# Optimization experiments

Hardware: AMD Instinct MI355X
Metric: run time of the kernel (lower is better)

The kernel has to match this reference:

```python
import jax, jax.numpy as jnp
import numpy as np

NUM_CLASSES = 10
GAMMA = 1.0
EPS = 1e-12


def setup_inputs() -> dict:
    key = jax.random.key(0)
    k1, k2, k3, k4 = jax.random.split(key, 4)
    x = jax.random.normal(k1, (1024, 64), dtype=jnp.float32)
    exemplars = jax.random.normal(k2, (50000, 64), dtype=jnp.float32)
    exemplar_labels = jax.random.randint(k3, (50000,), 0, NUM_CLASSES)
    # beta_raw initialized as softplus^{-1}(init_beta) with init_beta=1.0
    init_beta = 1.0
    beta_raw = jnp.array([np.log(np.exp(init_beta) - 1.0)], dtype=jnp.float32)
    return {"x": x, "exemplars": exemplars, "exemplar_labels": exemplar_labels,
            "beta_raw": beta_raw}


def reference(x, exemplars, exemplar_labels, beta_raw):
    # Squared Euclidean distances (weight_diag == ones) via GEMM expansion:
    # d2[b, e] = ||x_b||^2 + ||e_e||^2 - 2 <x_b, e_e>
    x2 = jnp.sum(x * x, axis=-1, keepdims=True)            # (B, 1)
    e2 = jnp.sum(exemplars * exemplars, axis=-1)           # (Ne,)
    d2 = x2 + e2[None, :] - 2.0 * (x @ exemplars.T)        # (B, Ne)
    d2 = jnp.maximum(d2, 0.0)  # true sq-dist is nonneg; guards GEMM round-off
    beta = jax.nn.softplus(beta_raw[0])
    sims = jnp.exp(-beta * d2)                              # (B, Ne)
    # scatter-add similarities into per-class bins: (C, B) -> (B, C)
    class_sims = jax.ops.segment_sum(sims.T, exemplar_labels,
                                     num_segments=NUM_CLASSES).T
    logits = GAMMA * jnp.log(class_sims + EPS)
    return logits
```

## Files before the change

### kernel.cpp

```cpp
#include <hip/hip_runtime.h>


#define NB      1024
#define NE      50000
#define NE_PAD  50176
#define NCHUNK  196
#define CROWS   256
#define KD      64
#define NC      10
#define SROWS   64
#define NSTAGE  4

using half8   = __attribute__((ext_vector_type(8))) _Float16;
using half4v  = __attribute__((ext_vector_type(4))) _Float16;
using floatx4 = __attribute__((ext_vector_type(4))) float;

__device__ __forceinline__ float softplus_f(float x) {
  return (x > 20.f) ? x : log1pf(__expf(x));
}

__global__ __launch_bounds__(256) void prep_kernel(
    const float* __restrict__ x, const float* __restrict__ ex,
    const int* __restrict__ labels, const float* __restrict__ beta_raw,
    _Float16* __restrict__ ex_h, float* __restrict__ ce,
    _Float16* __restrict__ x_h, float* __restrict__ cb,
    _Float16* __restrict__ oh_pre)
{
  const int tid = threadIdx.x;
  const float beta = softplus_f(beta_raw[0]);

  const int row = blockIdx.x * 16 + (tid >> 4);
  const int l16 = tid & 15;

  if (row < NE_PAD) {
    float4 v = make_float4(0.f, 0.f, 0.f, 0.f);
    if (row < NE) v = ((const float4*)ex)[row * 16 + l16];
    half4v hv = { (_Float16)v.x, (_Float16)v.y, (_Float16)v.z, (_Float16)v.w };
    *(half4v*)(ex_h + (size_t)row * KD + l16 * 4) = hv;
    float s = v.x*v.x + v.y*v.y + v.z*v.z + v.w*v.w;
    #pragma unroll
    for (int m = 1; m < 16; m <<= 1) s += __shfl_xor(s, m, 64);
    if (l16 == 0) ce[row] = (row < NE) ? (-beta * s) : -1e30f;
  } else {
    const int rx = row - NE_PAD;
    float4 v = ((const float4*)x)[rx * 16 + l16];
    half4v hv = { (_Float16)v.x, (_Float16)v.y, (_Float16)v.z, (_Float16)v.w };
    *(half4v*)(x_h + (size_t)rx * KD + l16 * 4) = hv;
    float s = v.x*v.x + v.y*v.y + v.z*v.z + v.w*v.w;
    #pragma unroll
    for (int m = 1; m < 16; m <<= 1) s += __shfl_xor(s, m, 64);
    if (l16 == 0) cb[rx] = -beta * s;
  }

  if (blockIdx.x < (NE_PAD / 16) && tid < 64) {
    const int l15  = tid & 15;
    const int quad = tid >> 4;
    const int base = min(blockIdx.x * 16 + quad * 4, NE - 4);
    const int4 lb = *(const int4*)(labels + base);
    half4v oh;
    oh[0] = (lb.x == l15) ? (_Float16)1.f : (_Float16)0.f;
    oh[1] = (lb.y == l15) ? (_Float16)1.f : (_Float16)0.f;
    oh[2] = (lb.z == l15) ? (_Float16)1.f : (_Float16)0.f;
    oh[3] = (lb.w == l15) ? (_Float16)1.f : (_Float16)0.f;
    ((half4v*)oh_pre)[blockIdx.x * 64 + tid] = oh;
  }
}

__global__ __launch_bounds__(256) void main_kernel(
    const _Float16* __restrict__ ex_h, const float* __restrict__ ce,
    const _Float16* __restrict__ x_h, const float* __restrict__ cb,
    const _Float16* __restrict__ oh_pre, const float* __restrict__ beta_raw,
    float* __restrict__ part)
{
  __shared__ _Float16 Ah[2][SROWS * KD];

  const int tid  = threadIdx.x;
  const int wave = tid >> 6;
  const int lane = tid & 63;
  const int l15  = lane & 15;
  const int quad = lane >> 4;

  const int btile = blockIdx.x;
  const int chunk = blockIdx.y;
  const int e0    = chunk * CROWS;
  const int bm    = btile * 128 + wave * 32;

  const float beta = softplus_f(beta_raw[0]);
  const float s2 = 2.f * beta;

  const half8* xr0 = (const half8*)(x_h + (size_t)(bm + l15) * KD);
  const half8* xr1 = (const half8*)(x_h + (size_t)(bm + 16 + l15) * KD);
  const half8 bx00 = xr0[quad];
  const half8 bx01 = xr0[quad + 4];
  const half8 bx10 = xr1[quad];
  const half8 bx11 = xr1[quad + 4];
  const float cbl0 = cb[bm + l15];
  const float cbl1 = cb[bm + 16 + l15];

  const int srow = tid >> 2;
  const int scol = tid & 3;
  const int ssw  = srow & 7;
  const _Float16* gsrc = ex_h + (size_t)(e0 + srow) * KD + scol * 16;
  const int lofs0 = srow * KD + (((2 * scol)     ^ ssw) * 8);
  const int lofs1 = srow * KD + (((2 * scol + 1) ^ ssw) * 8);

  half8 pr0 = *(const half8*)(gsrc);
  half8 pr1 = *(const half8*)(gsrc + 8);
  *(half8*)(&Ah[0][lofs0]) = pr0;
  *(half8*)(&Ah[0][lofs1]) = pr1;
  __syncthreads();

  floatx4 acc0 = {0.f, 0.f, 0.f, 0.f};
  floatx4 acc1 = {0.f, 0.f, 0.f, 0.f};

  const int rsw = l15 & 7;

  #pragma unroll
  for (int st = 0; st < NSTAGE; ++st) {
    const int b = st & 1;

    if (st + 1 < NSTAGE) {
      const _Float16* g = gsrc + (size_t)(st + 1) * SROWS * KD;
      pr0 = *(const half8*)(g);
      pr1 = *(const half8*)(g + 8);
    }

    float4 ce4s[4]; half4v ohs[4];
    #pragma unroll
    for (int sub = 0; sub < 4; ++sub) {
      ce4s[sub] = *(const float4*)(ce + e0 + st * SROWS + sub * 16 + quad * 4);
      ohs[sub]  = ((const half4v*)oh_pre)[(size_t)(chunk * 16 + st * 4 + sub) * 64 + lane];
    }

    #pragma unroll
    for (int sub = 0; sub < 4; ++sub) {
      const int rs = sub * 16 + l15;
      const half8 ae0 = *(const half8*)(&Ah[b][rs * KD + ((quad ^ rsw) * 8)]);
      const half8 ae1 = *(const half8*)(&Ah[b][rs * KD + (((quad + 4) ^ rsw) * 8)]);

      floatx4 d0 = {0.f, 0.f, 0.f, 0.f};
      d0 = __builtin_amdgcn_mfma_f32_16x16x32_f16(ae0, bx00, d0, 0, 0, 0);
      d0 = __builtin_amdgcn_mfma_f32_16x16x32_f16(ae1, bx01, d0, 0, 0, 0);
      floatx4 d1 = {0.f, 0.f, 0.f, 0.f};
      d1 = __builtin_amdgcn_mfma_f32_16x16x32_f16(ae0, bx10, d1, 0, 0, 0);
      d1 = __builtin_amdgcn_mfma_f32_16x16x32_f16(ae1, bx11, d1, 0, 0, 0);

      const float4 ce4 = ce4s[sub];
      const float cef[4] = { ce4.x, ce4.y, ce4.z, ce4.w };
      half4v p0, p1;
      #pragma unroll
      for (int r = 0; r < 4; ++r) {
        const float t0 = fminf(fmaf(s2, d0[r], cbl0 + cef[r]), 0.f);
        const float t1 = fminf(fmaf(s2, d1[r], cbl1 + cef[r]), 0.f);
        p0[r] = (_Float16)__expf(t0);
        p1[r] = (_Float16)__expf(t1);
      }

      acc0 = __builtin_amdgcn_mfma_f32_16x16x16f16(ohs[sub], p0, acc0, 0, 0, 0);
      acc1 = __builtin_amdgcn_mfma_f32_16x16x16f16(ohs[sub], p1, acc1, 0, 0, 0);
    }

    if (st + 1 < NSTAGE) {
      __syncthreads();
      const int nb = (st + 1) & 1;
      *(half8*)(&Ah[nb][lofs0]) = pr0;
      *(half8*)(&Ah[nb][lofs1]) = pr1;
      __syncthreads();
    }
  }

  float* dst = part + (size_t)chunk * (NB * NC);
  #pragma unroll
  for (int r = 0; r < 4; ++r) {
    const int c = quad * 4 + r;
    if (c < NC) {
      dst[(bm + l15) * NC + c]      = acc0[r];
      dst[(bm + 16 + l15) * NC + c] = acc1[r];
    }
  }
}

__global__ __launch_bounds__(256) void reduce_kernel(
    const float* __restrict__ part, float* __restrict__ out)
{
  const int bc = blockIdx.x * 256 + threadIdx.x;
  if (bc < NB * NC) {
    float s = 0.f;
    #pragma unroll 7
    for (int k = 0; k < NCHUNK; ++k) s += part[(size_t)k * (NB * NC) + bc];
    out[bc] = __logf(s + 1e-12f);
  }
}

extern "C" void kernel_launch(void* const* d_in, const int* in_sizes, int n_in,
                              void* d_out, int out_size, void* d_ws, size_t ws_size,
                              hipStream_t stream)
{
  const float* x        = (const float*)d_in[0];
  const float* ex       = (const float*)d_in[1];
  const int*   labels   = (const int*)d_in[2];
  const float* beta_raw = (const float*)d_in[3];
  float* out = (float*)d_out;

  char* ws = (char*)d_ws;
  _Float16* ex_h   = (_Float16*)ws;
  float*    ce     = (float*)(ws + 6422528);
  _Float16* x_h    = (_Float16*)(ws + 6623232);
  float*    cb     = (float*)(ws + 6754304);
  _Float16* oh_pre = (_Float16*)(ws + 6758400);
  float*    part   = (float*)(ws + 8364032);

  prep_kernel<<<3200, 256, 0, stream>>>(x, ex, labels, beta_raw,
                                        ex_h, ce, x_h, cb, oh_pre);
  dim3 g(8, 196);
  main_kernel<<<g, 256, 0, stream>>>(ex_h, ce, x_h, cb, oh_pre, beta_raw, part);
  reduce_kernel<<<40, 256, 0, stream>>>(part, out);
}
```

Before: 108.1 us.

## Load whole exemplar chunk to LDS once and widen per-wave batch tile

The main kernel now loads the full 256-row exemplar chunk, its norms and its one-hot labels into shared memory in a single pass with one barrier. The staged double-buffer loop and its per-stage barriers are gone. Each wave now covers 64 batch rows instead of 32, and the grid shrinks from 1568 to 784 blocks. This halves redundant exemplar reloads across batch tiles and removes synchronisation, at the cost of more registers, more LDS per block, fewer blocks and no load/compute overlap.

New measurement: 107.3 us. No clear change (-0.7%).

```diff
diff --git a/kernel.cpp b/kernel.cpp
--- a/kernel.cpp
+++ b/kernel.cpp
@@ -8,8 +8,6 @@
 #define CROWS   256
 #define KD      64
 #define NC      10
-#define SROWS   64
-#define NSTAGE  4
 
 using half8   = __attribute__((ext_vector_type(8))) _Float16;
 using half4v  = __attribute__((ext_vector_type(4))) _Float16;
@@ -72,7 +70,9 @@
     const _Float16* __restrict__ oh_pre, const float* __restrict__ beta_raw,
     float* __restrict__ part)
 {
-  __shared__ _Float16 Ah[2][SROWS * KD];
+  __shared__ _Float16 Ah[CROWS * KD];
+  __shared__ float    CeS[CROWS];
+  __shared__ _Float16 OhS[16 * 64 * 4];
 
   const int tid  = threadIdx.x;
   const int wave = tid >> 6;
@@ -80,102 +80,87 @@
   const int l15  = lane & 15;
   const int quad = lane >> 4;
 
-  const int btile = blockIdx.x;
-  const int chunk = blockIdx.y;
+  const int chunk = blockIdx.x >> 2;
+  const int grp   = blockIdx.x & 3;
   const int e0    = chunk * CROWS;
-  const int bm    = btile * 128 + wave * 32;
+  const int bmw   = grp * 256 + wave * 64;
 
   const float beta = softplus_f(beta_raw[0]);
   const float s2 = 2.f * beta;
 
-  const half8* xr0 = (const half8*)(x_h + (size_t)(bm + l15) * KD);
-  const half8* xr1 = (const half8*)(x_h + (size_t)(bm + 16 + l15) * KD);
-  const half8 bx00 = xr0[quad];
-  const half8 bx01 = xr0[quad + 4];
-  const half8 bx10 = xr1[quad];
-  const half8 bx11 = xr1[quad + 4];
-  const float cbl0 = cb[bm + l15];
-  const float cbl1 = cb[bm + 16 + l15];
-
   const int srow = tid >> 2;
   const int scol = tid & 3;
-  const int ssw  = srow & 7;
   const _Float16* gsrc = ex_h + (size_t)(e0 + srow) * KD + scol * 16;
-  const int lofs0 = srow * KD + (((2 * scol)     ^ ssw) * 8);
-  const int lofs1 = srow * KD + (((2 * scol + 1) ^ ssw) * 8);
-
-  half8 pr0 = *(const half8*)(gsrc);
-  half8 pr1 = *(const half8*)(gsrc + 8);
-  *(half8*)(&Ah[0][lofs0]) = pr0;
-  *(half8*)(&Ah[0][lofs1]) = pr1;
+  half8 r0[4], r1[4];
+  #pragma unroll
+  for (int p = 0; p < 4; ++p) {
+    r0[p] = *(const half8*)(gsrc + (size_t)p * 64 * KD);
+    r1[p] = *(const half8*)(gsrc + (size_t)p * 64 * KD + 8);
+  }
+  const float cev = ce[e0 + tid];
+  const int4* ohg = (const int4*)((const char*)oh_pre + (size_t)chunk * 8192 + tid * 32);
+  const int4 oha = ohg[0];
+  const int4 ohb = ohg[1];
+
+  half8 bx0[4], bx1[4];
+  float cbl[4];
+  #pragma unroll
+  for (int g2 = 0; g2 < 4; ++g2) {
+    const half8* xr = (const half8*)(x_h + (size_t)(bmw + g2 * 16 + l15) * KD);
+    bx0[g2] = xr[quad];
+    bx1[g2] = xr[quad + 4];
+    cbl[g2] = cb[bmw + g2 * 16 + l15];
+  }
+
+  const int ssw = srow & 7;
+  #pragma unroll
+  for (int p = 0; p < 4; ++p) {
+    const int rr = p * 64 + srow;
+    *(half8*)(&Ah[rr * KD + (((2 * scol)     ^ ssw) * 8)]) = r0[p];
+    *(half8*)(&Ah[rr * KD + (((2 * scol + 1) ^ ssw) * 8)]) = r1[p];
+  }
+  CeS[tid] = cev;
+  ((int4*)OhS)[tid * 2]     = oha;
+  ((int4*)OhS)[tid * 2 + 1] = ohb;
   __syncthreads();
 
-  floatx4 acc0 = {0.f, 0.f, 0.f, 0.f};
-  floatx4 acc1 = {0.f, 0.f, 0.f, 0.f};
-
+  floatx4 acc[4] = { {0,0,0,0}, {0,0,0,0}, {0,0,0,0}, {0,0,0,0} };
   const int rsw = l15 & 7;
 
-  #pragma unroll
-  for (int st = 0; st < NSTAGE; ++st) {
-    const int b = st & 1;
-
-    if (st + 1 < NSTAGE) {
-      const _Float16* g = gsrc + (size_t)(st + 1) * SROWS * KD;
-      pr0 = *(const half8*)(g);
-      pr1 = *(const half8*)(g + 8);
-    }
-
-    float4 ce4s[4]; half4v ohs[4];
-    #pragma unroll
-    for (int sub = 0; sub < 4; ++sub) {
-      ce4s[sub] = *(const float4*)(ce + e0 + st * SROWS + sub * 16 + quad * 4);
-      ohs[sub]  = ((const half4v*)oh_pre)[(size_t)(chunk * 16 + st * 4 + sub) * 64 + lane];
-    }
-
-    #pragma unroll
-    for (int sub = 0; sub < 4; ++sub) {
-      const int rs = sub * 16 + l15;
-      const half8 ae0 = *(const half8*)(&Ah[b][rs * KD + ((quad ^ rsw) * 8)]);
-      const half8 ae1 = *(const half8*)(&Ah[b][rs * KD + (((quad + 4) ^ rsw) * 8)]);
-
-      floatx4 d0 = {0.f, 0.f, 0.f, 0.f};
-      d0 = __builtin_amdgcn_mfma_f32_16x16x32_f16(ae0, bx00, d0, 0, 0, 0);
-      d0 = __builtin_amdgcn_mfma_f32_16x16x32_f16(ae1, bx01, d0, 0, 0, 0);
-      floatx4 d1 = {0.f, 0.f, 0.f, 0.f};
-      d1 = __builtin_amdgcn_mfma_f32_16x16x32_f16(ae0, bx10, d1, 0, 0, 0);
-      d1 = __builtin_amdgcn_mfma_f32_16x16x32_f16(ae1, bx11, d1, 0, 0, 0);
-
-      const float4 ce4 = ce4s[sub];
-      const float cef[4] = { ce4.x, ce4.y, ce4.z, ce4.w };
-      half4v p0, p1;
+  #pragma unroll 4
+  for (int rsub = 0; rsub < 16; ++rsub) {
+    const int rs = rsub * 16 + l15;
+    const half8 ae0 = *(const half8*)(&Ah[rs * KD + ((quad ^ rsw) * 8)]);
+    const half8 ae1 = *(const half8*)(&Ah[rs * KD + (((quad + 4) ^ rsw) * 8)]);
+    const float4 ce4 = *(const float4*)(&CeS[rsub * 16 + quad * 4]);
+    const half4v oh  = ((const half4v*)OhS)[rsub * 64 + lane];
+    const float cef[4] = { ce4.x, ce4.y, ce4.z, ce4.w };
+
+    #pragma unroll
+    for (int g2 = 0; g2 < 4; ++g2) {
+      floatx4 d = {0.f, 0.f, 0.f, 0.f};
+      d = __builtin_amdgcn_mfma_f32_16x16x32_f16(ae0, bx0[g2], d, 0, 0, 0);
+      d = __builtin_amdgcn_mfma_f32_16x16x32_f16(ae1, bx1[g2], d, 0, 0, 0);
+
+      half4v p;
       #pragma unroll
       for (int r = 0; r < 4; ++r) {
-        const float t0 = fminf(fmaf(s2, d0[r], cbl0 + cef[r]), 0.f);
-        const float t1 = fminf(fmaf(s2, d1[r], cbl1 + cef[r]), 0.f);
-        p0[r] = (_Float16)__expf(t0);
-        p1[r] = (_Float16)__expf(t1);
+        const float t = fminf(fmaf(s2, d[r], cbl[g2] + cef[r]), 0.f);
+        p[r] = (_Float16)__expf(t);
       }
-
-      acc0 = __builtin_amdgcn_mfma_f32_16x16x16f16(ohs[sub], p0, acc0, 0, 0, 0);
-      acc1 = __builtin_amdgcn_mfma_f32_16x16x16f16(ohs[sub], p1, acc1, 0, 0, 0);
+      acc[g2] = __builtin_amdgcn_mfma_f32_16x16x16f16(oh, p, acc[g2], 0, 0, 0);
     }
-
-    if (st + 1 < NSTAGE) {
-      __syncthreads();
-      const int nb = (st + 1) & 1;
-      *(half8*)(&Ah[nb][lofs0]) = pr0;
-      *(half8*)(&Ah[nb][lofs1]) = pr1;
-      __syncthreads();
-    }
   }
 
   float* dst = part + (size_t)chunk * (NB * NC);
   #pragma unroll
-  for (int r = 0; r < 4; ++r) {
-    const int c = quad * 4 + r;
-    if (c < NC) {
-      dst[(bm + l15) * NC + c]      = acc0[r];
-      dst[(bm + 16 + l15) * NC + c] = acc1[r];
+  for (int g2 = 0; g2 < 4; ++g2) {
+    #pragma unroll
+    for (int r = 0; r < 4; ++r) {
+      const int c = quad * 4 + r;
+      if (c < NC) {
+        dst[(bmw + g2 * 16 + l15) * NC + c] = acc[g2][r];
+      }
     }
   }
 }
@@ -212,7 +197,6 @@
 
   prep_kernel<<<3200, 256, 0, stream>>>(x, ex, labels, beta_raw,
                                         ex_h, ce, x_h, cb, oh_pre);
-  dim3 g(8, 196);
-  main_kernel<<<g, 256, 0, stream>>>(ex_h, ce, x_h, cb, oh_pre, beta_raw, part);
+  main_kernel<<<784, 256, 0, stream>>>(ex_h, ce, x_h, cb, oh_pre, beta_raw, part);
   reduce_kernel<<<40, 256, 0, stream>>>(part, out);
 }
```
